# Kernel optimization log

Measured on AMD Instinct MI355X. Metric: run time of the kernel, lower is better.

The kernel has to match this reference:

```python
import jax, jax.numpy as jnp
import numpy as np

PAD_ID = 50256  # GPT-J eos token used as pad


def setup_inputs() -> dict:
    key = jax.random.key(0)
    k1, k2, k3, k4 = jax.random.split(key, 4)
    B, S, D = 4, 2048, 4096  # B preference pairs -> 2B rows
    hidden_states = jax.random.normal(k1, (2 * B, S, D), dtype=jnp.float32)
    v_head_w = jax.random.normal(k2, (D,), dtype=jnp.float32) / np.sqrt(D).astype(np.float32)
    # tokens in [1, PAD_ID) so PAD only appears where we place it
    chosen = jax.random.randint(k3, (B, S), 1, PAD_ID)
    rejected = jax.random.randint(k4, (B, S), 1, PAD_ID)
    PROMPT = 512  # shared prompt so divergence_ind > 0
    rejected = rejected.at[:, :PROMPT].set(chosen[:, :PROMPT])
    pos = jnp.arange(S)[None, :]
    chosen = jnp.where(pos >= 1536, PAD_ID, chosen)     # chosen padded from 1536
    rejected = jnp.where(pos >= 1792, PAD_ID, rejected)  # rejected padded from 1792
    input_ids = jnp.concatenate([chosen, rejected], axis=0).astype(jnp.int64)
    return {"hidden_states": hidden_states, "v_head_w": v_head_w, "input_ids": input_ids}


def _first_index(mask, default):
    # index of first True along last axis, else `default`
    return jnp.where(mask.any(axis=-1), jnp.argmax(mask, axis=-1), default)


def reference(hidden_states, v_head_w, input_ids):
    # v_head: Linear(D, 1, bias=False) then squeeze(-1)
    rewards = jnp.einsum('bsd,d->bs', hidden_states, v_head_w)  # [2B, S]
    bs = input_ids.shape[0] // 2
    S = input_ids.shape[1]
    chosen, rejected = input_ids[:bs], input_ids[bs:]
    c_rew, r_rew = rewards[:bs], rewards[bs:]

    div_ind = _first_index(chosen != rejected, S)       # first divergence per pair
    c_ind = _first_index(chosen == PAD_ID, S)           # first pad (or S)
    r_ind = _first_index(rejected == PAD_ID, S)
    end_ind = jnp.maximum(c_ind, r_ind)

    pos = jnp.arange(S)[None, :]                         # [1, S]
    mask = (pos >= div_ind[:, None]) & (pos < end_ind[:, None])  # truncation window
    cnt = jnp.maximum(mask.sum(axis=-1), 1).astype(rewards.dtype)

    chosen_mean_scores = jnp.sum(jnp.where(mask, c_rew, 0.0), axis=-1) / cnt
    rejected_mean_scores = jnp.sum(jnp.where(mask, r_rew, 0.0), axis=-1) / cnt
    last = (end_ind - 1)[:, None]
    chosen_end_scores = jnp.take_along_axis(c_rew, last, axis=1)[:, 0]
    rejected_end_scores = jnp.take_along_axis(r_rew, last, axis=1)[:, 0]

    # -log(sigmoid(c - r)) averaged over the truncated window, then over pairs
    per_tok = -jax.nn.log_sigmoid(c_rew - r_rew)
    per_sample = jnp.sum(jnp.where(mask, per_tok, 0.0), axis=-1) / cnt
    loss = per_sample.mean()

    return loss, rewards, chosen_mean_scores, rejected_mean_scores, chosen_end_scores, rejected_end_scores
```

## Files before the change

### kernel.cpp

```cpp
#include <hip/hip_runtime.h>
#include <hip/hip_bf16.h>
#include <math.h>

#define PAD_ID 50256
#define S_LEN 2048
#define B_PAIRS 4
#define D4_C 1024
#define ROWS_PER_WAVE 2

__global__ __launch_bounds__(256) void rewards_kernel(
    const float4* __restrict__ hs,
    const float4* __restrict__ w4,
    float* __restrict__ rew,
    int nrows)
{
    const int wave = threadIdx.x >> 6;
    const int lane = threadIdx.x & 63;
    const int row0 = (blockIdx.x * 4 + wave) * ROWS_PER_WAVE;

    float4 wv[16];
    #pragma unroll
    for (int k = 0; k < 16; ++k)
        wv[k] = w4[lane + 64 * k];

    #pragma unroll
    for (int r = 0; r < ROWS_PER_WAVE; ++r) {
        const int row = row0 + r;
        if (row >= nrows) return;
        const float4* rp = hs + (size_t)row * D4_C;

        float acc0 = 0.0f, acc1 = 0.0f;
        #pragma unroll
        for (int k = 0; k < 16; k += 2) {
            float4 a0 = rp[lane + 64 * k];
            float4 a1 = rp[lane + 64 * (k + 1)];
            acc0 = fmaf(a0.x, wv[k].x, acc0);
            acc0 = fmaf(a0.y, wv[k].y, acc0);
            acc0 = fmaf(a0.z, wv[k].z, acc0);
            acc0 = fmaf(a0.w, wv[k].w, acc0);
            acc1 = fmaf(a1.x, wv[k + 1].x, acc1);
            acc1 = fmaf(a1.y, wv[k + 1].y, acc1);
            acc1 = fmaf(a1.z, wv[k + 1].z, acc1);
            acc1 = fmaf(a1.w, wv[k + 1].w, acc1);
        }
        float acc = acc0 + acc1;

        #pragma unroll
        for (int off = 32; off > 0; off >>= 1)
            acc += __shfl_down(acc, off, 64);
        if (lane == 0) rew[row] = acc;
    }
}

__device__ inline float wave_sum(float v) {
    #pragma unroll
    for (int off = 32; off > 0; off >>= 1) v += __shfl_down(v, off, 64);
    return v;
}
__device__ inline int wave_min(int v) {
    #pragma unroll
    for (int off = 32; off > 0; off >>= 1) v = min(v, __shfl_down(v, off, 64));
    return v;
}

__global__ __launch_bounds__(256) void scores_kernel(
    const float* __restrict__ rew,
    const int*   __restrict__ ids,
    float* __restrict__ out)
{
    __shared__ int   si[3][4];
    __shared__ float sf[3][4];
    __shared__ int   s_div, s_end;
    __shared__ float s_loss;

    const int tid  = threadIdx.x;
    const int lane = tid & 63;
    const int wave = tid >> 6;

    if (tid == 0) s_loss = 0.0f;
    __syncthreads();

    for (int b = 0; b < B_PAIRS; ++b) {
        const int*   ch = ids + (size_t)b * S_LEN;
        const int*   rj = ids + (size_t)(B_PAIRS + b) * S_LEN;
        const float* cr = rew + (size_t)b * S_LEN;
        const float* rr = rew + (size_t)(B_PAIRS + b) * S_LEN;

        int ldiv = S_LEN, lc = S_LEN, lr = S_LEN;
        for (int s = tid; s < S_LEN; s += 256) {
            int c = ch[s], r = rj[s];
            if (c != r)      ldiv = min(ldiv, s);
            if (c == PAD_ID) lc   = min(lc, s);
            if (r == PAD_ID) lr   = min(lr, s);
        }
        ldiv = wave_min(ldiv); lc = wave_min(lc); lr = wave_min(lr);
        if (lane == 0) { si[0][wave] = ldiv; si[1][wave] = lc; si[2][wave] = lr; }
        __syncthreads();
        if (tid == 0) {
            int dv = min(min(si[0][0], si[0][1]), min(si[0][2], si[0][3]));
            int ci = min(min(si[1][0], si[1][1]), min(si[1][2], si[1][3]));
            int ri = min(min(si[2][0], si[2][1]), min(si[2][2], si[2][3]));
            s_div = dv;
            s_end = max(ci, ri);
        }
        __syncthreads();
        const int dv = s_div, en = s_end;

        float sc = 0.0f, sr = 0.0f, sl = 0.0f;
        for (int s = dv + tid; s < en; s += 256) {
            float cv = cr[s], rv = rr[s];
            sc += cv;
            sr += rv;
            float x = cv - rv;
            sl += fmaxf(-x, 0.0f) + log1pf(expf(-fabsf(x)));
        }
        sc = wave_sum(sc); sr = wave_sum(sr); sl = wave_sum(sl);
        if (lane == 0) { sf[0][wave] = sc; sf[1][wave] = sr; sf[2][wave] = sl; }
        __syncthreads();
        if (tid == 0) {
            float tsc = sf[0][0] + sf[0][1] + sf[0][2] + sf[0][3];
            float tsr = sf[1][0] + sf[1][1] + sf[1][2] + sf[1][3];
            float tsl = sf[2][0] + sf[2][1] + sf[2][2] + sf[2][3];
            int cnt_i = en - dv;
            if (cnt_i < 1) cnt_i = 1;
            float inv_cnt = 1.0f / (float)cnt_i;
            int last = en - 1;
            if (last < 0) last = 0;
            const int base = 1 + 2 * B_PAIRS * S_LEN;
            out[base + 0 * B_PAIRS + b] = tsc * inv_cnt;
            out[base + 1 * B_PAIRS + b] = tsr * inv_cnt;
            out[base + 2 * B_PAIRS + b] = cr[last];
            out[base + 3 * B_PAIRS + b] = rr[last];
            s_loss += tsl * inv_cnt;
        }
        __syncthreads();
    }
    if (tid == 0) out[0] = s_loss / (float)B_PAIRS;
}

extern "C" void kernel_launch(void* const* d_in, const int* in_sizes, int n_in,
                              void* d_out, int out_size, void* d_ws, size_t ws_size,
                              hipStream_t stream) {
    const float* hs  = (const float*)d_in[0];
    const float* w   = (const float*)d_in[1];
    const int*   ids = (const int*)d_in[2];

    float* out = (float*)d_out;
    float* rew = out + 1;

    const int nrows = in_sizes[0] / in_sizes[1];

    const int rows_per_block = 4 * ROWS_PER_WAVE;
    const int blocks = (nrows + rows_per_block - 1) / rows_per_block;
    rewards_kernel<<<blocks, 256, 0, stream>>>(
        (const float4*)hs, (const float4*)w, rew, nrows);

    scores_kernel<<<1, 256, 0, stream>>>(rew, ids, out);
}
```

Measured before the change: 382.1 us.

## Fuse rewards and scoring kernels using a last-block atomic counter

```diff
diff --git a/kernel.cpp b/kernel.cpp
--- a/kernel.cpp
+++ b/kernel.cpp
@@ -6,136 +6,126 @@
 #define S_LEN 2048
 #define B_PAIRS 4
 #define D4_C 1024
-#define ROWS_PER_WAVE 2
 
-__global__ __launch_bounds__(256) void rewards_kernel(
+
+__device__ inline float wave_sum_xor(float v) {
+    #pragma unroll
+    for (int off = 32; off > 0; off >>= 1) v += __shfl_xor(v, off, 64);
+    return v;
+}
+__device__ inline int wave_min_xor(int v) {
+    #pragma unroll
+    for (int off = 32; off > 0; off >>= 1) v = min(v, __shfl_xor(v, off, 64));
+    return v;
+}
+
+__global__ __launch_bounds__(256) void fused_kernel(
     const float4* __restrict__ hs,
     const float4* __restrict__ w4,
-    float* __restrict__ rew,
+    const int*    __restrict__ ids,
+    float*        __restrict__ out,
+    unsigned*     __restrict__ ws,
     int nrows)
 {
+    float* rew = out + 1;
     const int wave = threadIdx.x >> 6;
     const int lane = threadIdx.x & 63;
-    const int row0 = (blockIdx.x * 4 + wave) * ROWS_PER_WAVE;
+    const int row0 = (blockIdx.x * 4 + wave) * 2;
 
     float4 wv[16];
     #pragma unroll
-    for (int k = 0; k < 16; ++k)
-        wv[k] = w4[lane + 64 * k];
+    for (int k = 0; k < 16; ++k) wv[k] = w4[lane + 64 * k];
 
     #pragma unroll
-    for (int r = 0; r < ROWS_PER_WAVE; ++r) {
+    for (int r = 0; r < 2; ++r) {
         const int row = row0 + r;
-        if (row >= nrows) return;
-        const float4* rp = hs + (size_t)row * D4_C;
+        if (row < nrows) {
+            const float4* rp = hs + (size_t)row * D4_C;
+            float acc0 = 0.0f, acc1 = 0.0f;
+            #pragma unroll
+            for (int k = 0; k < 16; k += 2) {
+                float4 a0 = rp[lane + 64 * k];
+                float4 a1 = rp[lane + 64 * (k + 1)];
+                acc0 = fmaf(a0.x, wv[k].x,     acc0);
+                acc0 = fmaf(a0.y, wv[k].y,     acc0);
+                acc0 = fmaf(a0.z, wv[k].z,     acc0);
+                acc0 = fmaf(a0.w, wv[k].w,     acc0);
+                acc1 = fmaf(a1.x, wv[k + 1].x, acc1);
+                acc1 = fmaf(a1.y, wv[k + 1].y, acc1);
+                acc1 = fmaf(a1.z, wv[k + 1].z, acc1);
+                acc1 = fmaf(a1.w, wv[k + 1].w, acc1);
+            }
+            float acc = acc0 + acc1;
+            #pragma unroll
+            for (int off = 32; off > 0; off >>= 1)
+                acc += __shfl_down(acc, off, 64);
+            if (lane == 0) rew[row] = acc;
+        }
+    }
 
-        float acc0 = 0.0f, acc1 = 0.0f;
-        #pragma unroll
-        for (int k = 0; k < 16; k += 2) {
-            float4 a0 = rp[lane + 64 * k];
-            float4 a1 = rp[lane + 64 * (k + 1)];
-            acc0 = fmaf(a0.x, wv[k].x, acc0);
-            acc0 = fmaf(a0.y, wv[k].y, acc0);
-            acc0 = fmaf(a0.z, wv[k].z, acc0);
-            acc0 = fmaf(a0.w, wv[k].w, acc0);
-            acc1 = fmaf(a1.x, wv[k + 1].x, acc1);
-            acc1 = fmaf(a1.y, wv[k + 1].y, acc1);
-            acc1 = fmaf(a1.z, wv[k + 1].z, acc1);
-            acc1 = fmaf(a1.w, wv[k + 1].w, acc1);
-        }
-        float acc = acc0 + acc1;
-
-        #pragma unroll
-        for (int off = 32; off > 0; off >>= 1)
-            acc += __shfl_down(acc, off, 64);
-        if (lane == 0) rew[row] = acc;
-    }
-}
-
-__device__ inline float wave_sum(float v) {
-    #pragma unroll
-    for (int off = 32; off > 0; off >>= 1) v += __shfl_down(v, off, 64);
-    return v;
-}
-__device__ inline int wave_min(int v) {
-    #pragma unroll
-    for (int off = 32; off > 0; off >>= 1) v = min(v, __shfl_down(v, off, 64));
-    return v;
-}
-
-__global__ __launch_bounds__(256) void scores_kernel(
-    const float* __restrict__ rew,
-    const int*   __restrict__ ids,
-    float* __restrict__ out)
-{
-    __shared__ int   si[3][4];
-    __shared__ float sf[3][4];
-    __shared__ int   s_div, s_end;
-    __shared__ float s_loss;
-
-    const int tid  = threadIdx.x;
-    const int lane = tid & 63;
-    const int wave = tid >> 6;
-
-    if (tid == 0) s_loss = 0.0f;
-    __syncthreads();
-
-    for (int b = 0; b < B_PAIRS; ++b) {
-        const int*   ch = ids + (size_t)b * S_LEN;
-        const int*   rj = ids + (size_t)(B_PAIRS + b) * S_LEN;
-        const float* cr = rew + (size_t)b * S_LEN;
-        const float* rr = rew + (size_t)(B_PAIRS + b) * S_LEN;
-
+    if (blockIdx.x == 0) {
+        const int b = wave;
+        const int* ch = ids + b * S_LEN;
+        const int* rj = ids + (B_PAIRS + b) * S_LEN;
         int ldiv = S_LEN, lc = S_LEN, lr = S_LEN;
-        for (int s = tid; s < S_LEN; s += 256) {
+        for (int s = lane; s < S_LEN; s += 64) {
             int c = ch[s], r = rj[s];
             if (c != r)      ldiv = min(ldiv, s);
             if (c == PAD_ID) lc   = min(lc, s);
             if (r == PAD_ID) lr   = min(lr, s);
         }
-        ldiv = wave_min(ldiv); lc = wave_min(lc); lr = wave_min(lr);
-        if (lane == 0) { si[0][wave] = ldiv; si[1][wave] = lc; si[2][wave] = lr; }
-        __syncthreads();
-        if (tid == 0) {
-            int dv = min(min(si[0][0], si[0][1]), min(si[0][2], si[0][3]));
-            int ci = min(min(si[1][0], si[1][1]), min(si[1][2], si[1][3]));
-            int ri = min(min(si[2][0], si[2][1]), min(si[2][2], si[2][3]));
-            s_div = dv;
-            s_end = max(ci, ri);
+        ldiv = wave_min_xor(ldiv);
+        lc   = wave_min_xor(lc);
+        lr   = wave_min_xor(lr);
+        if (lane == 0) {
+            ws[2 + 2 * b] = (unsigned)ldiv;
+            ws[3 + 2 * b] = (unsigned)max(lc, lr);
         }
-        __syncthreads();
-        const int dv = s_div, en = s_end;
+    }
 
+    __threadfence();
+    __syncthreads();
+    __shared__ bool is_last;
+    if (threadIdx.x == 0)
+        is_last = (atomicAdd(ws, 1u) == (unsigned)(gridDim.x - 1));
+    __syncthreads();
+    if (!is_last) return;
+    __threadfence();
+
+    __shared__ float s_loss[B_PAIRS];
+    {
+        const int b  = wave;
+        const int dv = (int)ws[2 + 2 * b];
+        const int en = (int)ws[3 + 2 * b];
+        const float* cr = rew + b * S_LEN;
+        const float* rr = rew + (B_PAIRS + b) * S_LEN;
         float sc = 0.0f, sr = 0.0f, sl = 0.0f;
-        for (int s = dv + tid; s < en; s += 256) {
+        for (int s = dv + lane; s < en; s += 64) {
             float cv = cr[s], rv = rr[s];
             sc += cv;
             sr += rv;
             float x = cv - rv;
             sl += fmaxf(-x, 0.0f) + log1pf(expf(-fabsf(x)));
         }
-        sc = wave_sum(sc); sr = wave_sum(sr); sl = wave_sum(sl);
-        if (lane == 0) { sf[0][wave] = sc; sf[1][wave] = sr; sf[2][wave] = sl; }
-        __syncthreads();
-        if (tid == 0) {
-            float tsc = sf[0][0] + sf[0][1] + sf[0][2] + sf[0][3];
-            float tsr = sf[1][0] + sf[1][1] + sf[1][2] + sf[1][3];
-            float tsl = sf[2][0] + sf[2][1] + sf[2][2] + sf[2][3];
-            int cnt_i = en - dv;
-            if (cnt_i < 1) cnt_i = 1;
-            float inv_cnt = 1.0f / (float)cnt_i;
-            int last = en - 1;
-            if (last < 0) last = 0;
+        sc = wave_sum_xor(sc);
+        sr = wave_sum_xor(sr);
+        sl = wave_sum_xor(sl);
+        if (lane == 0) {
+            int   cnt = max(en - dv, 1);
+            float inv = 1.0f / (float)cnt;
+            int  last = max(en - 1, 0);
             const int base = 1 + 2 * B_PAIRS * S_LEN;
-            out[base + 0 * B_PAIRS + b] = tsc * inv_cnt;
-            out[base + 1 * B_PAIRS + b] = tsr * inv_cnt;
+            out[base + 0 * B_PAIRS + b] = sc * inv;
+            out[base + 1 * B_PAIRS + b] = sr * inv;
             out[base + 2 * B_PAIRS + b] = cr[last];
             out[base + 3 * B_PAIRS + b] = rr[last];
-            s_loss += tsl * inv_cnt;
+            s_loss[b] = sl * inv;
         }
-        __syncthreads();
     }
-    if (tid == 0) out[0] = s_loss / (float)B_PAIRS;
+    __syncthreads();
+    if (threadIdx.x == 0)
+        out[0] = (s_loss[0] + s_loss[1] + s_loss[2] + s_loss[3]) *
+                 (1.0f / (float)B_PAIRS);
 }
 
 extern "C" void kernel_launch(void* const* d_in, const int* in_sizes, int n_in,
@@ -145,15 +135,15 @@
     const float* w   = (const float*)d_in[1];
     const int*   ids = (const int*)d_in[2];
 
-    float* out = (float*)d_out;
-    float* rew = out + 1;
+    float*    out = (float*)d_out;
+    unsigned* ws  = (unsigned*)d_ws;
 
     const int nrows = in_sizes[0] / in_sizes[1];
+    const int rows_per_block = 4 * 2;
+    const int blocks = (nrows + rows_per_block - 1) / rows_per_block;
 
-    const int rows_per_block = 4 * ROWS_PER_WAVE;
-    const int blocks = (nrows + rows_per_block - 1) / rows_per_block;
-    rewards_kernel<<<blocks, 256, 0, stream>>>(
-        (const float4*)hs, (const float4*)w, rew, nrows);
+    hipMemsetAsync(ws, 0, sizeof(unsigned), stream);
 
-    scores_kernel<<<1, 256, 0, stream>>>(rew, ids, out);
+    fused_kernel<<<blocks, 256, 0, stream>>>(
+        (const float4*)hs, (const float4*)w, ids, out, ws, nrows);
 }
```

Result: slower. 672.0 us (+75.9%).
